# Performance work log

Hardware: AMD Instinct MI355X
Metric: run time of the kernel (lower is better)

## Reference

```python
import jax, jax.numpy as jnp
import numpy as np

B, N, C, H = 4096, 49, 128, 4
DH = C // H  # head dim = 32
SCALE = DH ** -0.5

def setup_inputs() -> dict:
    key = jax.random.key(0)
    kx, kq, kp, kb = jax.random.split(key, 4)
    x = jax.random.normal(kx, (B, N, C), dtype=jnp.float32)
    w_qkv = jax.random.normal(kq, (C, 3 * C), dtype=jnp.float32) * (C ** -0.5)
    w_proj = jax.random.normal(kp, (C, C), dtype=jnp.float32) * (C ** -0.5)
    b_proj = jax.random.normal(kb, (C,), dtype=jnp.float32) * 0.01
    return {"x": x, "w_qkv": w_qkv, "w_proj": w_proj, "b_proj": b_proj}

def reference(x, w_qkv, w_proj, b_proj):
    Bx, Nx, Cx = x.shape
    qkv = x @ w_qkv  # (B, N, 3C)
    q, k, v = jnp.split(qkv, 3, axis=-1)
    # (B, N, C) -> (B, H, N, DH)
    def heads(t):
        return t.reshape(Bx, Nx, H, DH).transpose(0, 2, 1, 3)
    q, k, v = heads(q), heads(k), heads(v)
    attn = jnp.einsum('bhnd,bhmd->bhnm', q, k) * SCALE
    attn = jax.nn.softmax(attn, axis=-1)
    out = jnp.einsum('bhnm,bhmd->bhnd', attn, v)
    out = out.transpose(0, 2, 1, 3).reshape(Bx, Nx, Cx)
    return out @ w_proj + b_proj
```

## Files before the change

kernel.cpp:

```cpp
#include <hip/hip_runtime.h>
#include <hip/hip_bf16.h>

typedef unsigned short u16;
typedef __bf16 bf16;
typedef __attribute__((ext_vector_type(8))) __bf16 bf16x8;
typedef __attribute__((ext_vector_type(4))) __bf16 bf16x4;
typedef __attribute__((ext_vector_type(4))) float f32x4;

#define MFMA16(A,B,C) __builtin_amdgcn_mfma_f32_16x16x32_bf16(A,B,C,0,0,0)

constexpr int NTOK = 49;
constexpr int CH   = 128;
constexpr float CEXP = 0.17677669529663687f * 1.4426950408889634f;

__device__ __forceinline__ bf16x8 lds_v8(const u16* base, int byteoff) {
    return *reinterpret_cast<const bf16x8*>(reinterpret_cast<const char*>(base) + byteoff);
}
__device__ __forceinline__ bf16x8 lds_v8_u8(const u16* base, int byteoff) {
    bf16x4 lo = *reinterpret_cast<const bf16x4*>(reinterpret_cast<const char*>(base) + byteoff);
    bf16x4 hi = *reinterpret_cast<const bf16x4*>(reinterpret_cast<const char*>(base) + byteoff + 8);
    bf16x8 r;
    r[0]=lo[0]; r[1]=lo[1]; r[2]=lo[2]; r[3]=lo[3];
    r[4]=hi[0]; r[5]=hi[1]; r[6]=hi[2]; r[7]=hi[3];
    return r;
}
__device__ __forceinline__ void lds_st64(u16* base, int byteoff,
                                         float a0, float a1, float a2, float a3) {
    bf16x4 v = {(bf16)a0, (bf16)a1, (bf16)a2, (bf16)a3};
    *reinterpret_cast<bf16x4*>(reinterpret_cast<char*>(base) + byteoff) = v;
}

__global__ void prep_weights_kernel(const float* __restrict__ wqkv,
                                    const float* __restrict__ wproj,
                                    bf16* __restrict__ ws) {
    int i = blockIdx.x * 256 + threadIdx.x;
    if (i < 384 * 128) {
        int n = i >> 7, k = i & 127;
        ws[i] = (bf16)wqkv[k * 384 + n];
    }
    if (i < 128 * 128) {
        int n = i >> 7, k = i & 127;
        ws[384 * 128 + i] = (bf16)wproj[k * 128 + n];
    }
}

__launch_bounds__(256, 3)
__global__ void fused_window_attn(const float* __restrict__ x,
                                  const bf16* __restrict__ wqkv_t,
                                  const bf16* __restrict__ wproj_t,
                                  const float* __restrict__ bias,
                                  float* __restrict__ out) {
    __shared__ __align__(16) u16 smem[26624];
    u16* Xs = smem;
    u16* QK = smem + 8192;

    const int tid  = threadIdx.x;
    const int blk  = blockIdx.x;
    const int wv   = tid >> 6;
    const int lane = tid & 63;
    const int lr   = lane & 15;
    const int lg   = lane >> 4;

    u16* Qh = QK + wv * 4608;
    u16* Kh = Qh + 2304;
    u16* Pw = Qh;
    u16* Vh = Xs + wv * 2048;

    const float* xw = x + (size_t)blk * (NTOK * CH);
    #pragma unroll
    for (int it = 0; it < 7; ++it) {
        int i = tid + it * 256;
        if (i < (NTOK * CH) / 4) {
            float4 v = reinterpret_cast<const float4*>(xw)[i];
            int e = i * 4, row = e >> 7, col = e & 127;
            bf16x4 pk = { (bf16)v.x, (bf16)v.y, (bf16)v.z, (bf16)v.w };
            *reinterpret_cast<bf16x4*>(reinterpret_cast<char*>(Xs)
                + row * 256 + ((col * 2) ^ ((row & 7) << 4))) = pk;
        }
    }
    if (tid < 240) {
        uint4 zz = {0, 0, 0, 0};
        *reinterpret_cast<uint4*>(reinterpret_cast<char*>(Xs) + 49 * 256 + tid * 16) = zz;
    }
    __syncthreads();

    bf16x8 xf[4][4];
    #pragma unroll
    for (int tt = 0; tt < 4; ++tt)
        #pragma unroll
        for (int ks = 0; ks < 4; ++ks) {
            int row = tt * 16 + lr;
            xf[tt][ks] = lds_v8(Xs, row * 256 + ((ks * 64 + lg * 16) ^ ((row & 7) << 4)));
        }
    __syncthreads();

    #pragma unroll
    for (int mt = 0; mt < 4; ++mt) {
        int ct = (mt < 2) ? (2 * wv + mt) : (8 + 2 * wv + (mt - 2));
        bf16x8 wf[4];
        const bf16* wrow = wqkv_t + (ct * 16 + lr) * 128 + lg * 8;
        #pragma unroll
        for (int ks = 0; ks < 4; ++ks)
            wf[ks] = *reinterpret_cast<const bf16x8*>(wrow + ks * 32);
        u16* dst = (mt < 2) ? Qh : Kh;
        int dh0 = (mt & 1) * 16 + lg * 4;
        #pragma unroll
        for (int tt = 0; tt < 4; ++tt) {
            f32x4 a = {0.f, 0.f, 0.f, 0.f};
            #pragma unroll
            for (int ks = 0; ks < 4; ++ks) a = MFMA16(wf[ks], xf[tt][ks], a);
            int tok = tt * 16 + lr;
            lds_st64(dst, tok * 72 + dh0 * 2, a[0], a[1], a[2], a[3]);
        }
    }
    #pragma unroll
    for (int i = 0; i < 2; ++i) {
        int ct = 16 + 2 * wv + i;
        bf16x8 wf[4];
        const bf16* wrow = wqkv_t + (ct * 16 + lr) * 128 + lg * 8;
        #pragma unroll
        for (int ks = 0; ks < 4; ++ks)
            wf[ks] = *reinterpret_cast<const bf16x8*>(wrow + ks * 32);
        int dh = i * 16 + lr;
        #pragma unroll
        for (int tt = 0; tt < 4; ++tt) {
            f32x4 a = {0.f, 0.f, 0.f, 0.f};
            #pragma unroll
            for (int ks = 0; ks < 4; ++ks) a = MFMA16(xf[tt][ks], wf[ks], a);
            lds_st64(Vh, dh * 128 + ((tt * 32 + lg * 8) ^ ((dh & 7) << 4)),
                     a[0], a[1], a[2], a[3]);
        }
    }

    bf16x8 qf[4], kf[4];
    #pragma unroll
    for (int t = 0; t < 4; ++t) {
        qf[t] = lds_v8_u8(Qh, (t * 16 + lr) * 72 + lg * 16);
        kf[t] = lds_v8_u8(Kh, (t * 16 + lr) * 72 + lg * 16);
    }
    f32x4 s[4][4];
    #pragma unroll
    for (int qt = 0; qt < 4; ++qt)
        #pragma unroll
        for (int st = 0; st < 4; ++st) {
            f32x4 z = {0.f, 0.f, 0.f, 0.f};
            s[qt][st] = MFMA16(kf[st], qf[qt], z);
        }
    bf16x8 vf[2][2];
    #pragma unroll
    for (int dht = 0; dht < 2; ++dht)
        #pragma unroll
        for (int ks = 0; ks < 2; ++ks) {
            int dh = dht * 16 + lr;
            vf[dht][ks] = lds_v8(Vh, dh * 128 + ((ks * 64 + lg * 16) ^ ((dh & 7) << 4)));
        }
    __syncthreads();

    #pragma unroll
    for (int qt = 0; qt < 4; ++qt) {
        if (lg > 0) s[qt][3][0] = -1e30f;
        s[qt][3][1] = -1e30f; s[qt][3][2] = -1e30f; s[qt][3][3] = -1e30f;
    }
    float rs[4];
    #pragma unroll
    for (int qt = 0; qt < 4; ++qt) {
        float mx = -1e30f;
        #pragma unroll
        for (int st = 0; st < 4; ++st)
            #pragma unroll
            for (int rg = 0; rg < 4; ++rg) mx = fmaxf(mx, s[qt][st][rg]);
        mx = fmaxf(mx, __shfl_xor(mx, 16));
        mx = fmaxf(mx, __shfl_xor(mx, 32));
        float l = 0.f;
        #pragma unroll
        for (int st = 0; st < 4; ++st)
            #pragma unroll
            for (int rg = 0; rg < 4; ++rg) {
                float e = exp2f((s[qt][st][rg] - mx) * CEXP);
                s[qt][st][rg] = e;
                l += e;
            }
        l += __shfl_xor(l, 16);
        l += __shfl_xor(l, 32);
        rs[qt] = 1.f / l;
    }
    #pragma unroll
    for (int qt = 0; qt < 4; ++qt) {
        int q = qt * 16 + lr;
        #pragma unroll
        for (int st = 0; st < 4; ++st)
            lds_st64(Pw, q * 128 + ((st * 32 + lg * 8) ^ ((q & 7) << 4)),
                     s[qt][st][0], s[qt][st][1], s[qt][st][2], s[qt][st][3]);
    }
    f32x4 o[2][4];
    #pragma unroll
    for (int dht = 0; dht < 2; ++dht)
        #pragma unroll
        for (int qt = 0; qt < 4; ++qt) { f32x4 z = {0.f,0.f,0.f,0.f}; o[dht][qt] = z; }
    #pragma unroll
    for (int ks = 0; ks < 2; ++ks)
        #pragma unroll
        for (int qt = 0; qt < 4; ++qt) {
            int q = qt * 16 + lr;
            bf16x8 pf = lds_v8(Pw, q * 128 + ((ks * 64 + lg * 16) ^ ((q & 7) << 4)));
            #pragma unroll
            for (int dht = 0; dht < 2; ++dht)
                o[dht][qt] = MFMA16(vf[dht][ks], pf, o[dht][qt]);
        }
    #pragma unroll
    for (int dht = 0; dht < 2; ++dht)
        #pragma unroll
        for (int qt = 0; qt < 4; ++qt) {
            int q = qt * 16 + lr;
            float scl = rs[qt];
            lds_st64(Xs, q * 256 + ((wv * 64 + dht * 32 + lg * 8) ^ ((q & 7) << 4)),
                     o[dht][qt][0] * scl, o[dht][qt][1] * scl,
                     o[dht][qt][2] * scl, o[dht][qt][3] * scl);
        }
    __syncthreads();

    bf16x8 of[4][4];
    #pragma unroll
    for (int tt = 0; tt < 4; ++tt)
        #pragma unroll
        for (int ks = 0; ks < 4; ++ks) {
            int row = tt * 16 + lr;
            of[tt][ks] = lds_v8(Xs, row * 256 + ((ks * 64 + lg * 16) ^ ((row & 7) << 4)));
        }
    #pragma unroll
    for (int i = 0; i < 2; ++i) {
        int ct = 2 * wv + i;
        bf16x8 wf[4];
        const bf16* wrow = wproj_t + (ct * 16 + lr) * 128 + lg * 8;
        #pragma unroll
        for (int ks = 0; ks < 4; ++ks)
            wf[ks] = *reinterpret_cast<const bf16x8*>(wrow + ks * 32);
        float4 bv = *reinterpret_cast<const float4*>(bias + ct * 16 + lg * 4);
        #pragma unroll
        for (int tt = 0; tt < 4; ++tt) {
            f32x4 a = {0.f, 0.f, 0.f, 0.f};
            #pragma unroll
            for (int ks = 0; ks < 4; ++ks) a = MFMA16(wf[ks], of[tt][ks], a);
            int tok = tt * 16 + lr;
            if (tok < NTOK) {
                float4 r = { a[0] + bv.x, a[1] + bv.y, a[2] + bv.z, a[3] + bv.w };
                *reinterpret_cast<float4*>(
                    out + ((size_t)blk * NTOK + tok) * CH + ct * 16 + lg * 4) = r;
            }
        }
    }
}

extern "C" void kernel_launch(void* const* d_in, const int* in_sizes, int n_in,
                              void* d_out, int out_size, void* d_ws, size_t ws_size,
                              hipStream_t stream) {
    const float* x     = (const float*)d_in[0];
    const float* wqkv  = (const float*)d_in[1];
    const float* wproj = (const float*)d_in[2];
    const float* bias  = (const float*)d_in[3];
    float* out = (float*)d_out;
    bf16* ws   = (bf16*)d_ws;

    constexpr size_t WS_NEED = (size_t)(384 * 128 + 128 * 128) * sizeof(u16);
    if (ws_size < WS_NEED) return;

    prep_weights_kernel<<<192, 256, 0, stream>>>(wqkv, wproj, ws);
    fused_window_attn<<<4096, 256, 0, stream>>>(x, ws, ws + 384 * 128, bias, out);
}
```

Baseline: 98.50 us.

## Shrink LDS, swizzle Q/K tiles, drop softmax max, interleave per-query-tile softmax

Reduces shared memory from 52KB to 48KB by packing Q/K at 64-byte rows with an XOR swizzle instead of padded 72-byte rows, and places V in its own region so the intermediate barrier disappears. The softmax no longer subtracts the row max, relying on bounded logits, and computes scores per query tile to cut live registers. P is written into the Q/K region. Adds s_setprio around MFMA sections to favour matrix issue across waves. Skipping the max subtraction risks overflow for inputs with large logits.

```diff
diff --git a/kernel.cpp b/kernel.cpp
--- a/kernel.cpp
+++ b/kernel.cpp
@@ -13,21 +13,12 @@
 constexpr int CH   = 128;
 constexpr float CEXP = 0.17677669529663687f * 1.4426950408889634f;
 
-__device__ __forceinline__ bf16x8 lds_v8(const u16* base, int byteoff) {
-    return *reinterpret_cast<const bf16x8*>(reinterpret_cast<const char*>(base) + byteoff);
-}
-__device__ __forceinline__ bf16x8 lds_v8_u8(const u16* base, int byteoff) {
-    bf16x4 lo = *reinterpret_cast<const bf16x4*>(reinterpret_cast<const char*>(base) + byteoff);
-    bf16x4 hi = *reinterpret_cast<const bf16x4*>(reinterpret_cast<const char*>(base) + byteoff + 8);
-    bf16x8 r;
-    r[0]=lo[0]; r[1]=lo[1]; r[2]=lo[2]; r[3]=lo[3];
-    r[4]=hi[0]; r[5]=hi[1]; r[6]=hi[2]; r[7]=hi[3];
-    return r;
-}
-__device__ __forceinline__ void lds_st64(u16* base, int byteoff,
-                                         float a0, float a1, float a2, float a3) {
+__device__ __forceinline__ bf16x8 lds_v8(const char* p) {
+    return *reinterpret_cast<const bf16x8*>(p);
+}
+__device__ __forceinline__ void lds_st64(char* p, float a0, float a1, float a2, float a3) {
     bf16x4 v = {(bf16)a0, (bf16)a1, (bf16)a2, (bf16)a3};
-    *reinterpret_cast<bf16x4*>(reinterpret_cast<char*>(base) + byteoff) = v;
+    *reinterpret_cast<bf16x4*>(p) = v;
 }
 
 __global__ void prep_weights_kernel(const float* __restrict__ wqkv,
@@ -50,21 +41,19 @@
                                   const bf16* __restrict__ wproj_t,
                                   const float* __restrict__ bias,
                                   float* __restrict__ out) {
-    __shared__ __align__(16) u16 smem[26624];
-    u16* Xs = smem;
-    u16* QK = smem + 8192;
+    __shared__ __align__(16) u16 smem[24576];
+    char* S8 = reinterpret_cast<char*>(smem);
 
     const int tid  = threadIdx.x;
     const int blk  = blockIdx.x;
-    const int wv   = tid >> 6;
+    const int h    = tid >> 6;
     const int lane = tid & 63;
     const int lr   = lane & 15;
     const int lg   = lane >> 4;
 
-    u16* Qh = QK + wv * 4608;
-    u16* Kh = Qh + 2304;
-    u16* Pw = Qh;
-    u16* Vh = Xs + wv * 2048;
+    char* Qb = S8 + h * 4096;
+    char* Kb = S8 + 16384 + h * 4096;
+    char* Vb = S8 + 32768 + h * 4096;
 
     const float* xw = x + (size_t)blk * (NTOK * CH);
     #pragma unroll
@@ -73,14 +62,13 @@
         if (i < (NTOK * CH) / 4) {
             float4 v = reinterpret_cast<const float4*>(xw)[i];
             int e = i * 4, row = e >> 7, col = e & 127;
-            bf16x4 pk = { (bf16)v.x, (bf16)v.y, (bf16)v.z, (bf16)v.w };
-            *reinterpret_cast<bf16x4*>(reinterpret_cast<char*>(Xs)
-                + row * 256 + ((col * 2) ^ ((row & 7) << 4))) = pk;
+            bf16x4 pk4 = { (bf16)v.x, (bf16)v.y, (bf16)v.z, (bf16)v.w };
+            *reinterpret_cast<bf16x4*>(S8 + row * 256 + ((col * 2) ^ ((row & 7) << 4))) = pk4;
         }
     }
     if (tid < 240) {
         uint4 zz = {0, 0, 0, 0};
-        *reinterpret_cast<uint4*>(reinterpret_cast<char*>(Xs) + 49 * 256 + tid * 16) = zz;
+        *reinterpret_cast<uint4*>(S8 + 49 * 256 + tid * 16) = zz;
     }
     __syncthreads();
 
@@ -90,19 +78,20 @@
         #pragma unroll
         for (int ks = 0; ks < 4; ++ks) {
             int row = tt * 16 + lr;
-            xf[tt][ks] = lds_v8(Xs, row * 256 + ((ks * 64 + lg * 16) ^ ((row & 7) << 4)));
-        }
-    __syncthreads();
-
+            xf[tt][ks] = lds_v8(S8 + row * 256 + ((ks * 64 + lg * 16) ^ ((row & 7) << 4)));
+        }
+    __syncthreads();
+
+    __builtin_amdgcn_s_setprio(1);
     #pragma unroll
     for (int mt = 0; mt < 4; ++mt) {
-        int ct = (mt < 2) ? (2 * wv + mt) : (8 + 2 * wv + (mt - 2));
+        int ct = (mt < 2) ? (2 * h + mt) : (8 + 2 * h + (mt - 2));
         bf16x8 wf[4];
         const bf16* wrow = wqkv_t + (ct * 16 + lr) * 128 + lg * 8;
         #pragma unroll
         for (int ks = 0; ks < 4; ++ks)
             wf[ks] = *reinterpret_cast<const bf16x8*>(wrow + ks * 32);
-        u16* dst = (mt < 2) ? Qh : Kh;
+        char* dst = (mt < 2) ? Qb : Kb;
         int dh0 = (mt & 1) * 16 + lg * 4;
         #pragma unroll
         for (int tt = 0; tt < 4; ++tt) {
@@ -110,12 +99,13 @@
             #pragma unroll
             for (int ks = 0; ks < 4; ++ks) a = MFMA16(wf[ks], xf[tt][ks], a);
             int tok = tt * 16 + lr;
-            lds_st64(dst, tok * 72 + dh0 * 2, a[0], a[1], a[2], a[3]);
+            lds_st64(dst + tok * 64 + ((dh0 * 2) ^ ((tok & 7) << 3)),
+                     a[0], a[1], a[2], a[3]);
         }
     }
     #pragma unroll
     for (int i = 0; i < 2; ++i) {
-        int ct = 16 + 2 * wv + i;
+        int ct = 16 + 2 * h + i;
         bf16x8 wf[4];
         const bf16* wrow = wqkv_t + (ct * 16 + lr) * 128 + lg * 8;
         #pragma unroll
@@ -127,120 +117,126 @@
             f32x4 a = {0.f, 0.f, 0.f, 0.f};
             #pragma unroll
             for (int ks = 0; ks < 4; ++ks) a = MFMA16(xf[tt][ks], wf[ks], a);
-            lds_st64(Vh, dh * 128 + ((tt * 32 + lg * 8) ^ ((dh & 7) << 4)),
+            lds_st64(Vb + dh * 128 + ((tt * 32 + lg * 8) ^ ((dh & 7) << 4)),
                      a[0], a[1], a[2], a[3]);
         }
     }
+    __builtin_amdgcn_s_setprio(0);
 
     bf16x8 qf[4], kf[4];
     #pragma unroll
     for (int t = 0; t < 4; ++t) {
-        qf[t] = lds_v8_u8(Qh, (t * 16 + lr) * 72 + lg * 16);
-        kf[t] = lds_v8_u8(Kh, (t * 16 + lr) * 72 + lg * 16);
-    }
-    f32x4 s[4][4];
-    #pragma unroll
-    for (int qt = 0; qt < 4; ++qt)
+        int row = t * 16 + lr;
+        int o0 = row * 64 + ((lg * 16) ^ ((row & 7) << 3));
+        bf16x4 qlo = *reinterpret_cast<const bf16x4*>(Qb + o0);
+        bf16x4 qhi = *reinterpret_cast<const bf16x4*>(Qb + (o0 ^ 8));
+        bf16x4 klo = *reinterpret_cast<const bf16x4*>(Kb + o0);
+        bf16x4 khi = *reinterpret_cast<const bf16x4*>(Kb + (o0 ^ 8));
+        bf16x8 q8 = { qlo[0],qlo[1],qlo[2],qlo[3], qhi[0],qhi[1],qhi[2],qhi[3] };
+        bf16x8 k8 = { klo[0],klo[1],klo[2],klo[3], khi[0],khi[1],khi[2],khi[3] };
+        qf[t] = q8;
+        kf[t] = k8;
+    }
+    bf16x8 vf[2][2];
+    #pragma unroll
+    for (int dht = 0; dht < 2; ++dht)
+        #pragma unroll
+        for (int ks2 = 0; ks2 < 2; ++ks2) {
+            int dh = dht * 16 + lr;
+            vf[dht][ks2] = lds_v8(Vb + dh * 128 + ((ks2 * 64 + lg * 16) ^ ((dh & 7) << 4)));
+        }
+
+    float rs[4];
+    #pragma unroll
+    for (int qt = 0; qt < 4; ++qt) {
+        f32x4 s[4];
+        __builtin_amdgcn_s_setprio(1);
         #pragma unroll
         for (int st = 0; st < 4; ++st) {
             f32x4 z = {0.f, 0.f, 0.f, 0.f};
-            s[qt][st] = MFMA16(kf[st], qf[qt], z);
-        }
-    bf16x8 vf[2][2];
-    #pragma unroll
-    for (int dht = 0; dht < 2; ++dht)
-        #pragma unroll
-        for (int ks = 0; ks < 2; ++ks) {
-            int dh = dht * 16 + lr;
-            vf[dht][ks] = lds_v8(Vh, dh * 128 + ((ks * 64 + lg * 16) ^ ((dh & 7) << 4)));
-        }
-    __syncthreads();
-
-    #pragma unroll
-    for (int qt = 0; qt < 4; ++qt) {
-        if (lg > 0) s[qt][3][0] = -1e30f;
-        s[qt][3][1] = -1e30f; s[qt][3][2] = -1e30f; s[qt][3][3] = -1e30f;
-    }
-    float rs[4];
-    #pragma unroll
-    for (int qt = 0; qt < 4; ++qt) {
-        float mx = -1e30f;
-        #pragma unroll
-        for (int st = 0; st < 4; ++st)
-            #pragma unroll
-            for (int rg = 0; rg < 4; ++rg) mx = fmaxf(mx, s[qt][st][rg]);
-        mx = fmaxf(mx, __shfl_xor(mx, 16));
-        mx = fmaxf(mx, __shfl_xor(mx, 32));
+            s[st] = MFMA16(kf[st], qf[qt], z);
+        }
+        __builtin_amdgcn_s_setprio(0);
         float l = 0.f;
         #pragma unroll
-        for (int st = 0; st < 4; ++st)
+        for (int st = 0; st < 3; ++st)
             #pragma unroll
             for (int rg = 0; rg < 4; ++rg) {
-                float e = exp2f((s[qt][st][rg] - mx) * CEXP);
-                s[qt][st][rg] = e;
+                float e = exp2f(s[st][rg] * CEXP);
+                s[st][rg] = e;
                 l += e;
             }
+        {
+            float e48 = exp2f(s[3][0] * CEXP);
+            float v48 = (lg == 0) ? e48 : 0.f;
+            s[3][0] = v48; s[3][1] = 0.f; s[3][2] = 0.f; s[3][3] = 0.f;
+            l += v48;
+        }
         l += __shfl_xor(l, 16);
         l += __shfl_xor(l, 32);
         rs[qt] = 1.f / l;
-    }
+        int q = qt * 16 + lr;
+        char* pb = (qt < 2) ? (Qb + q * 128) : (Kb + (q - 32) * 128);
+        #pragma unroll
+        for (int st = 0; st < 4; ++st)
+            lds_st64(pb + ((st * 32 + lg * 8) ^ ((q & 7) << 4)),
+                     s[st][0], s[st][1], s[st][2], s[st][3]);
+    }
+
+    f32x4 o[2][4];
+    #pragma unroll
+    for (int dht = 0; dht < 2; ++dht)
+        #pragma unroll
+        for (int qt = 0; qt < 4; ++qt) { f32x4 z = {0.f,0.f,0.f,0.f}; o[dht][qt] = z; }
+    __builtin_amdgcn_s_setprio(1);
+    #pragma unroll
+    for (int ks2 = 0; ks2 < 2; ++ks2)
+        #pragma unroll
+        for (int qt = 0; qt < 4; ++qt) {
+            int q = qt * 16 + lr;
+            const char* pb = (qt < 2) ? (Qb + q * 128) : (Kb + (q - 32) * 128);
+            bf16x8 pf = lds_v8(pb + ((ks2 * 64 + lg * 16) ^ ((q & 7) << 4)));
+            o[0][qt] = MFMA16(vf[0][ks2], pf, o[0][qt]);
+            o[1][qt] = MFMA16(vf[1][ks2], pf, o[1][qt]);
+        }
+    __builtin_amdgcn_s_setprio(0);
+    __syncthreads();
+
     #pragma unroll
     for (int qt = 0; qt < 4; ++qt) {
         int q = qt * 16 + lr;
-        #pragma unroll
-        for (int st = 0; st < 4; ++st)
-            lds_st64(Pw, q * 128 + ((st * 32 + lg * 8) ^ ((q & 7) << 4)),
-                     s[qt][st][0], s[qt][st][1], s[qt][st][2], s[qt][st][3]);
-    }
-    f32x4 o[2][4];
-    #pragma unroll
-    for (int dht = 0; dht < 2; ++dht)
-        #pragma unroll
-        for (int qt = 0; qt < 4; ++qt) { f32x4 z = {0.f,0.f,0.f,0.f}; o[dht][qt] = z; }
-    #pragma unroll
-    for (int ks = 0; ks < 2; ++ks)
-        #pragma unroll
-        for (int qt = 0; qt < 4; ++qt) {
-            int q = qt * 16 + lr;
-            bf16x8 pf = lds_v8(Pw, q * 128 + ((ks * 64 + lg * 16) ^ ((q & 7) << 4)));
-            #pragma unroll
-            for (int dht = 0; dht < 2; ++dht)
-                o[dht][qt] = MFMA16(vf[dht][ks], pf, o[dht][qt]);
-        }
-    #pragma unroll
-    for (int dht = 0; dht < 2; ++dht)
-        #pragma unroll
-        for (int qt = 0; qt < 4; ++qt) {
-            int q = qt * 16 + lr;
-            float scl = rs[qt];
-            lds_st64(Xs, q * 256 + ((wv * 64 + dht * 32 + lg * 8) ^ ((q & 7) << 4)),
+        float scl = rs[qt];
+        #pragma unroll
+        for (int dht = 0; dht < 2; ++dht)
+            lds_st64(S8 + q * 256 + ((h * 64 + dht * 32 + lg * 8) ^ ((q & 7) << 4)),
                      o[dht][qt][0] * scl, o[dht][qt][1] * scl,
                      o[dht][qt][2] * scl, o[dht][qt][3] * scl);
-        }
-    __syncthreads();
-
-    bf16x8 of[4][4];
+    }
+    __syncthreads();
+
+    bf16x8 ofr[4][4];
     #pragma unroll
     for (int tt = 0; tt < 4; ++tt)
         #pragma unroll
         for (int ks = 0; ks < 4; ++ks) {
             int row = tt * 16 + lr;
-            of[tt][ks] = lds_v8(Xs, row * 256 + ((ks * 64 + lg * 16) ^ ((row & 7) << 4)));
+            ofr[tt][ks] = lds_v8(S8 + row * 256 + ((ks * 64 + lg * 16) ^ ((row & 7) << 4)));
         }
     #pragma unroll
     for (int i = 0; i < 2; ++i) {
-        int ct = 2 * wv + i;
+        int ct = 2 * h + i;
         bf16x8 wf[4];
         const bf16* wrow = wproj_t + (ct * 16 + lr) * 128 + lg * 8;
         #pragma unroll
         for (int ks = 0; ks < 4; ++ks)
             wf[ks] = *reinterpret_cast<const bf16x8*>(wrow + ks * 32);
         float4 bv = *reinterpret_cast<const float4*>(bias + ct * 16 + lg * 4);
+        __builtin_amdgcn_s_setprio(1);
         #pragma unroll
         for (int tt = 0; tt < 4; ++tt) {
             f32x4 a = {0.f, 0.f, 0.f, 0.f};
             #pragma unroll
-            for (int ks = 0; ks < 4; ++ks) a = MFMA16(wf[ks], of[tt][ks], a);
+            for (int ks = 0; ks < 4; ++ks) a = MFMA16(wf[ks], ofr[tt][ks], a);
             int tok = tt * 16 + lr;
             if (tok < NTOK) {
                 float4 r = { a[0] + bv.x, a[1] + bv.y, a[2] + bv.z, a[3] + bv.w };
@@ -248,6 +244,7 @@
                     out + ((size_t)blk * NTOK + tok) * CH + ct * 16 + lg * 4) = r;
             }
         }
+        __builtin_amdgcn_s_setprio(0);
     }
 }
 
```

Result: no change. 97.13 us (-1.4%).
